# Kernel optimization log

Measured on AMD Instinct MI355X. Metric: run time of the kernel, lower is better.

The kernel has to match this reference:

```python
import jax, jax.numpy as jnp
import numpy as np

B, K, NS, NT = 4, 16, 4096, 16384
TEMPERATURE = 1.0


def setup_inputs() -> dict:
    key = jax.random.key(0)
    k1, k2, k3 = jax.random.split(key, 3)
    return {
        "sem_logits": jax.random.normal(k1, (B, K, NS), dtype=jnp.float32),
        "source_pos": jax.random.normal(k2, (B, 3, NS), dtype=jnp.float32),
        "target_pos": jax.random.normal(k3, (B, 3, NT), dtype=jnp.float32),
    }


def reference(sem_logits, source_pos, target_pos):
    # temperature scaling
    x = sem_logits / max(1e-06, TEMPERATURE)
    # use_max_class=True: per-point max over class logits -> [B, 1, Ns]
    src_feat = jnp.max(x, axis=1, keepdims=True)

    # nearest neighbor via squared euclidean distance (argmin matches cdist+top-1)
    t = jnp.swapaxes(target_pos, 1, 2)  # [B, Nt, 3]
    s = jnp.swapaxes(source_pos, 1, 2)  # [B, Ns, 3]
    d2 = (
        jnp.sum(t * t, axis=-1, keepdims=True)        # [B, Nt, 1]
        + jnp.sum(s * s, axis=-1)[:, None, :]          # [B, 1, Ns]
        - 2.0 * jnp.einsum("bnd,bmd->bnm", t, s)      # [B, Nt, Ns]
    )
    nn_idx = jnp.argmin(d2, axis=-1)  # [B, Nt]

    # gather: torch's source_feat[batch_idx, :, nn_idx] yields [B, Nt, C]
    gathered = jnp.take_along_axis(src_feat, nn_idx[:, None, :], axis=2)  # [B, 1, Nt]
    out = jnp.swapaxes(gathered, 1, 2)  # [B, Nt, 1]
    return jax.nn.sigmoid(out)
```

## Files before the change

kernel.cpp:

```cpp
#include <hip/hip_runtime.h>
#include <math.h>
#include <float.h>

#define BATCH 4
#define KCLS 16
#define NSRC 4096
#define NTGT 16384

#define THREADS 512
#define WAVES 8
#define TGT_PER_BLOCK 128
#define CHUNK 2048
#define NCHUNK (NSRC / CHUNK)
#define STRIPE (CHUNK / WAVES)

__global__ __launch_bounds__(THREADS) void fused_kernel(
    const float* __restrict__ sem_logits,
    const float* __restrict__ source_pos,
    const float* __restrict__ target_pos,
    float* __restrict__ out)
{
    __shared__ float4 ls[CHUNK];

    int tid = threadIdx.x;
    int lane = tid & 63;
    int wave = tid >> 6;

    const int blocksPerBatch = NTGT / TGT_PER_BLOCK;
    int b = blockIdx.x / blocksPerBatch;
    int tbase = (blockIdx.x - b * blocksPerBatch) * TGT_PER_BLOCK;

    const float* tp = target_pos + (size_t)b * 3 * NTGT;
    int t0 = tbase + lane, t1 = tbase + 64 + lane;
    float tx0 = tp[t0], ty0 = tp[NTGT + t0], tz0 = tp[2 * NTGT + t0];
    float tx1 = tp[t1], ty1 = tp[NTGT + t1], tz1 = tp[2 * NTGT + t1];
    float tt0 = __fadd_rn(__fadd_rn(__fmul_rn(tx0, tx0), __fmul_rn(ty0, ty0)),
                          __fmul_rn(tz0, tz0));
    float tt1 = __fadd_rn(__fadd_rn(__fmul_rn(tx1, tx1), __fmul_rn(ty1, ty1)),
                          __fmul_rn(tz1, tz1));

    const float* sx = source_pos + (size_t)b * 3 * NSRC;
    const float* sy = sx + NSRC;
    const float* sz = sx + 2 * NSRC;

    float best0 = FLT_MAX, best1 = FLT_MAX;
    int bi0 = 0, bi1 = 0;

    for (int c = 0; c < NCHUNK; ++c) {
        __syncthreads();
        int cg = c * CHUNK;
#pragma unroll
        for (int j = 0; j < CHUNK / THREADS; ++j) {
            int s = tid + j * THREADS;
            float x = sx[cg + s], y = sy[cg + s], z = sz[cg + s];
            float ss = __fadd_rn(__fadd_rn(__fmul_rn(x, x), __fmul_rn(y, y)),
                                 __fmul_rn(z, z));
            ls[s] = make_float4(x, y, z, ss);
        }
        __syncthreads();

        int lbase = wave * STRIPE;
        int gbase = cg + lbase;
#pragma unroll 8
        for (int i = 0; i < STRIPE; ++i) {
            float4 f = ls[lbase + i];
            float acc0 = __fmul_rn(tx0, f.x);
            acc0 = __fmaf_rn(ty0, f.y, acc0);
            acc0 = __fmaf_rn(tz0, f.z, acc0);
            float d20 = __fmaf_rn(-2.0f, acc0, __fadd_rn(tt0, f.w));
            if (d20 < best0) { best0 = d20; bi0 = gbase + i; }
            float acc1 = __fmul_rn(tx1, f.x);
            acc1 = __fmaf_rn(ty1, f.y, acc1);
            acc1 = __fmaf_rn(tz1, f.z, acc1);
            float d21 = __fmaf_rn(-2.0f, acc1, __fadd_rn(tt1, f.w));
            if (d21 < best1) { best1 = d21; bi1 = gbase + i; }
        }
    }

    __syncthreads();

    float* smin = (float*)ls;
    int* sidx = (int*)ls + WAVES * TGT_PER_BLOCK;
    smin[wave * TGT_PER_BLOCK + lane] = best0;
    sidx[wave * TGT_PER_BLOCK + lane] = bi0;
    smin[wave * TGT_PER_BLOCK + 64 + lane] = best1;
    sidx[wave * TGT_PER_BLOCK + 64 + lane] = bi1;
    __syncthreads();

    if (tid < TGT_PER_BLOCK) {
        float m = smin[tid];
        int mi = sidx[tid];
#pragma unroll
        for (int j = 1; j < WAVES; ++j) {
            float mj = smin[j * TGT_PER_BLOCK + tid];
            int ij = sidx[j * TGT_PER_BLOCK + tid];
            if (mj < m || (mj == m && ij < mi)) { m = mj; mi = ij; }
        }
        const float* lg = sem_logits + (size_t)b * KCLS * NSRC + mi;
        float mm = lg[0];
#pragma unroll
        for (int k = 1; k < KCLS; ++k) mm = fmaxf(mm, lg[(size_t)k * NSRC]);
        out[(size_t)b * NTGT + tbase + tid] = 1.0f / (1.0f + expf(-mm));
    }
}

extern "C" void kernel_launch(void* const* d_in, const int* in_sizes, int n_in,
                              void* d_out, int out_size, void* d_ws, size_t ws_size,
                              hipStream_t stream) {
    const float* sem_logits = (const float*)d_in[0];
    const float* source_pos = (const float*)d_in[1];
    const float* target_pos = (const float*)d_in[2];
    float* out = (float*)d_out;

    fused_kernel<<<BATCH * (NTGT / TGT_PER_BLOCK), THREADS, 0, stream>>>(
        sem_logits, source_pos, target_pos, out);
}
```

Before: 107.5 us.

## Split source range across blocks with packed 64-bit atomicMin reduction

Raises targets per thread from two to four to reuse each LDS source load across more distance evaluations, and splits the source points into four chunks handled by separate blocks. Partial argmin results are combined through a 64-bit atomicMin on an order-preserving float key packed with the index, and a separate gate kernel does the logit max and sigmoid. The goal is more reuse of each LDS read and a grid that is still large enough after the per-block target count doubles. The cost is a memset, an extra kernel launch and global atomics through the workspace.

```diff
diff --git a/kernel.cpp b/kernel.cpp
--- a/kernel.cpp
+++ b/kernel.cpp
@@ -9,16 +9,16 @@
 
 #define THREADS 512
 #define WAVES 8
-#define TGT_PER_BLOCK 128
-#define CHUNK 2048
-#define NCHUNK (NSRC / CHUNK)
+#define TPL 4
+#define TGT_PER_BLOCK 256
+#define SPLITS 4
+#define CHUNK (NSRC / SPLITS)
 #define STRIPE (CHUNK / WAVES)
 
-__global__ __launch_bounds__(THREADS) void fused_kernel(
-    const float* __restrict__ sem_logits,
+__global__ __launch_bounds__(THREADS, 8) void nn_partial_kernel(
     const float* __restrict__ source_pos,
     const float* __restrict__ target_pos,
-    float* __restrict__ out)
+    unsigned long long* __restrict__ ws64)
 {
     __shared__ float4 ls[CHUNK];
 
@@ -26,65 +26,68 @@
     int lane = tid & 63;
     int wave = tid >> 6;
 
-    const int blocksPerBatch = NTGT / TGT_PER_BLOCK;
-    int b = blockIdx.x / blocksPerBatch;
-    int tbase = (blockIdx.x - b * blocksPerBatch) * TGT_PER_BLOCK;
-
-    const float* tp = target_pos + (size_t)b * 3 * NTGT;
-    int t0 = tbase + lane, t1 = tbase + 64 + lane;
-    float tx0 = tp[t0], ty0 = tp[NTGT + t0], tz0 = tp[2 * NTGT + t0];
-    float tx1 = tp[t1], ty1 = tp[NTGT + t1], tz1 = tp[2 * NTGT + t1];
-    float tt0 = __fadd_rn(__fadd_rn(__fmul_rn(tx0, tx0), __fmul_rn(ty0, ty0)),
-                          __fmul_rn(tz0, tz0));
-    float tt1 = __fadd_rn(__fadd_rn(__fmul_rn(tx1, tx1), __fmul_rn(ty1, ty1)),
-                          __fmul_rn(tz1, tz1));
+    int b = blockIdx.x >> 8;
+    int rem = blockIdx.x & 255;
+    int tg = rem >> 2;
+    int split = rem & 3;
+    int tbase = tg * TGT_PER_BLOCK;
+    int cg = split * CHUNK;
 
     const float* sx = source_pos + (size_t)b * 3 * NSRC;
     const float* sy = sx + NSRC;
     const float* sz = sx + 2 * NSRC;
+#pragma unroll
+    for (int j = 0; j < CHUNK / THREADS; ++j) {
+        int s = tid + j * THREADS;
+        float x = sx[cg + s], y = sy[cg + s], z = sz[cg + s];
+        float ss = __fadd_rn(__fadd_rn(__fmul_rn(x, x), __fmul_rn(y, y)),
+                             __fmul_rn(z, z));
+        ls[s] = make_float4(x, y, z, ss);
+    }
 
-    float best0 = FLT_MAX, best1 = FLT_MAX;
-    int bi0 = 0, bi1 = 0;
+    const float* tp = target_pos + (size_t)b * 3 * NTGT;
+    float tx[TPL], ty[TPL], tz[TPL], tt[TPL];
+#pragma unroll
+    for (int j = 0; j < TPL; ++j) {
+        int t = tbase + 64 * j + lane;
+        tx[j] = tp[t]; ty[j] = tp[NTGT + t]; tz[j] = tp[2 * NTGT + t];
+        tt[j] = __fadd_rn(__fadd_rn(__fmul_rn(tx[j], tx[j]),
+                                    __fmul_rn(ty[j], ty[j])),
+                          __fmul_rn(tz[j], tz[j]));
+    }
 
-    for (int c = 0; c < NCHUNK; ++c) {
-        __syncthreads();
-        int cg = c * CHUNK;
+    __syncthreads();
+
+    int lbase = wave * STRIPE;
+    int gbase = cg + lbase;
+    float best[TPL];
+    int bi[TPL];
 #pragma unroll
-        for (int j = 0; j < CHUNK / THREADS; ++j) {
-            int s = tid + j * THREADS;
-            float x = sx[cg + s], y = sy[cg + s], z = sz[cg + s];
-            float ss = __fadd_rn(__fadd_rn(__fmul_rn(x, x), __fmul_rn(y, y)),
-                                 __fmul_rn(z, z));
-            ls[s] = make_float4(x, y, z, ss);
-        }
-        __syncthreads();
+    for (int j = 0; j < TPL; ++j) { best[j] = FLT_MAX; bi[j] = 0; }
 
-        int lbase = wave * STRIPE;
-        int gbase = cg + lbase;
 #pragma unroll 8
-        for (int i = 0; i < STRIPE; ++i) {
-            float4 f = ls[lbase + i];
-            float acc0 = __fmul_rn(tx0, f.x);
-            acc0 = __fmaf_rn(ty0, f.y, acc0);
-            acc0 = __fmaf_rn(tz0, f.z, acc0);
-            float d20 = __fmaf_rn(-2.0f, acc0, __fadd_rn(tt0, f.w));
-            if (d20 < best0) { best0 = d20; bi0 = gbase + i; }
-            float acc1 = __fmul_rn(tx1, f.x);
-            acc1 = __fmaf_rn(ty1, f.y, acc1);
-            acc1 = __fmaf_rn(tz1, f.z, acc1);
-            float d21 = __fmaf_rn(-2.0f, acc1, __fadd_rn(tt1, f.w));
-            if (d21 < best1) { best1 = d21; bi1 = gbase + i; }
+    for (int i = 0; i < STRIPE; ++i) {
+        float4 f = ls[lbase + i];
+        int cand = gbase + i;
+#pragma unroll
+        for (int j = 0; j < TPL; ++j) {
+            float acc = __fmul_rn(tx[j], f.x);
+            acc = __fmaf_rn(ty[j], f.y, acc);
+            acc = __fmaf_rn(tz[j], f.z, acc);
+            float d2 = __fmaf_rn(-2.0f, acc, __fadd_rn(tt[j], f.w));
+            if (d2 < best[j]) { best[j] = d2; bi[j] = cand; }
         }
     }
 
     __syncthreads();
 
     float* smin = (float*)ls;
-    int* sidx = (int*)ls + WAVES * TGT_PER_BLOCK;
-    smin[wave * TGT_PER_BLOCK + lane] = best0;
-    sidx[wave * TGT_PER_BLOCK + lane] = bi0;
-    smin[wave * TGT_PER_BLOCK + 64 + lane] = best1;
-    sidx[wave * TGT_PER_BLOCK + 64 + lane] = bi1;
+    int* sidx = (int*)(smin + WAVES * TGT_PER_BLOCK);
+#pragma unroll
+    for (int j = 0; j < TPL; ++j) {
+        smin[wave * TGT_PER_BLOCK + 64 * j + lane] = best[j];
+        sidx[wave * TGT_PER_BLOCK + 64 * j + lane] = bi[j];
+    }
     __syncthreads();
 
     if (tid < TGT_PER_BLOCK) {
@@ -96,12 +99,28 @@
             int ij = sidx[j * TGT_PER_BLOCK + tid];
             if (mj < m || (mj == m && ij < mi)) { m = mj; mi = ij; }
         }
-        const float* lg = sem_logits + (size_t)b * KCLS * NSRC + mi;
-        float mm = lg[0];
+        unsigned u = __float_as_uint(m);
+        unsigned ord = (u & 0x80000000u) ? ~u : (u | 0x80000000u);
+        unsigned long long packed =
+            ((unsigned long long)ord << 32) | (unsigned)mi;
+        atomicMin(&ws64[(size_t)b * NTGT + tbase + tid], packed);
+    }
+}
+
+__global__ __launch_bounds__(256) void gate_kernel(
+    const unsigned long long* __restrict__ ws64,
+    const float* __restrict__ sem_logits,
+    float* __restrict__ out)
+{
+    int gt = blockIdx.x * 256 + threadIdx.x;
+    int b = gt / NTGT;
+    int mi = (int)(ws64[gt] & 0xFFFFFFFFull);
+
+    const float* lg = sem_logits + (size_t)b * KCLS * NSRC + mi;
+    float mm = lg[0];
 #pragma unroll
-        for (int k = 1; k < KCLS; ++k) mm = fmaxf(mm, lg[(size_t)k * NSRC]);
-        out[(size_t)b * NTGT + tbase + tid] = 1.0f / (1.0f + expf(-mm));
-    }
+    for (int k = 1; k < KCLS; ++k) mm = fmaxf(mm, lg[(size_t)k * NSRC]);
+    out[gt] = 1.0f / (1.0f + expf(-mm));
 }
 
 extern "C" void kernel_launch(void* const* d_in, const int* in_sizes, int n_in,
@@ -112,6 +131,11 @@
     const float* target_pos = (const float*)d_in[2];
     float* out = (float*)d_out;
 
-    fused_kernel<<<BATCH * (NTGT / TGT_PER_BLOCK), THREADS, 0, stream>>>(
-        sem_logits, source_pos, target_pos, out);
+    unsigned long long* ws64 = (unsigned long long*)d_ws;
+
+    hipMemsetAsync(ws64, 0xFF, sizeof(unsigned long long) * BATCH * NTGT, stream);
+
+    nn_partial_kernel<<<BATCH * (NTGT / TGT_PER_BLOCK) * SPLITS, THREADS, 0, stream>>>(
+        source_pos, target_pos, ws64);
+    gate_kernel<<<(BATCH * NTGT) / 256, 256, 0, stream>>>(ws64, sem_logits, out);
 }
```

Result: faster. 102.5 us (-4.6%).
